# Optimization experiments

Hardware: AMD Instinct MI355X
Metric: run time of the kernel (lower is better)

The kernel has to match this reference:

```python
import jax, jax.numpy as jnp
import numpy as np

GRID = 16
PAD = 32
RADIUS = 8
SIGMA = 1.5
B = 8192
N_SEEDS = 24


def setup_inputs() -> dict:
    key = jax.random.key(0)
    k1, k2 = jax.random.split(key)
    # predicted seeds: (x, y, phase), coords in [0, GRID)
    output = jax.random.uniform(k1, (B, N_SEEDS * 3), dtype=jnp.float32) * GRID
    # target seeds: (x, y, amp), coords in [0, 2*GRID)
    targets = jax.random.uniform(k2, (B, N_SEEDS * 3), dtype=jnp.float32) * (2 * GRID)
    return {"output": output, "targets": targets}


def _forward(output, targets):
    Bn = output.shape[0]
    seeds = output.reshape(Bn, -1, 3)   # (B, N, 3): x, y, phase
    tgt = targets.reshape(Bn, -1, 3)    # (B, M, 3): x, y, amp

    # --- discrete Voronoi on GRID x GRID (vectorized over batch) ---
    c = jnp.arange(GRID, dtype=output.dtype)
    xx, yy = jnp.meshgrid(c, c, indexing='ij')  # (GRID, GRID)
    dist = jnp.sqrt((xx[None, :, :, None] - seeds[:, None, None, :, 0]) ** 2
                    + (yy[None, :, :, None] - seeds[:, None, None, :, 1]) ** 2)
    labels = jnp.argmin(dist, axis=-1)  # (B, GRID, GRID) int

    # circular support on the inner grid (np.ogrid[-r:r, -r:r] convention)
    cc = jnp.arange(-RADIUS, RADIUS)
    inner = (cc[:, None] ** 2 + cc[None, :] ** 2) <= RADIUS ** 2
    labels = jnp.where(inner[None], labels, 0)

    # zero-pad voronoi labels to PAD x PAD
    pw = (PAD - GRID) // 2
    padded = jnp.pad(labels, ((0, 0), (pw, pw), (pw, pw)))  # (B, PAD, PAD)

    # --- gather phase per pixel, zero outside circle on padded grid ---
    phases = seeds[:, :, 2]  # (B, N)
    phase = jnp.take_along_axis(phases, padded.reshape(Bn, -1), axis=1).reshape(Bn, PAD, PAD)
    pc = jnp.arange(PAD)
    center = PAD // 2
    outside = (pc[:, None] - center) ** 2 + (pc[None, :] - center) ** 2 > RADIUS ** 2
    phase = jnp.where(outside[None], jnp.zeros_like(phase), phase)

    # --- density = amp(=1) * exp(i * 2*pi * phase), shifted FFT magnitude ---
    two_pi = 2.0 * jnp.pi
    density = jax.lax.complex(jnp.cos(two_pi * phase), jnp.sin(two_pi * phase))
    pred = jnp.fft.fftshift(density, axes=(-2, -1))
    pred = jnp.fft.fft2(pred)
    pred_dp = jnp.abs(jnp.fft.fftshift(pred, axes=(-2, -1)))  # (B, PAD, PAD)

    # --- target diffraction: sum of Gaussians on (2*GRID)x(2*GRID) grid ---
    xc = jnp.arange(PAD, dtype=targets.dtype)  # height == width == 2*GRID == PAD
    tx = tgt[:, :, 0][:, :, None, None]
    ty = tgt[:, :, 1][:, :, None, None]
    amp = tgt[:, :, 2][:, :, None, None]
    # torch: x varies along last axis, y along second-to-last
    d2 = (xc[None, None, None, :] - tx) ** 2 + (xc[None, None, :, None] - ty) ** 2
    tgt_dp = jnp.sum(amp * jnp.exp(-d2 / (2.0 * SIGMA ** 2)), axis=1)  # (B, PAD, PAD)

    # --- chi-square (global max-normalization and reductions) ---
    p = pred_dp / jnp.max(pred_dp)
    t = tgt_dp / jnp.max(tgt_dp)
    return jnp.sum((p - t) ** 2) / jnp.sqrt(jnp.sum(p ** 2) * jnp.sum(t ** 2))


def reference(output, targets):
    return _forward(output, targets)
```

## Files before the change

kernel.cpp:

```cpp
#include <hip/hip_runtime.h>
#include <math.h>

#define NS 24

typedef float v2f __attribute__((ext_vector_type(2)));
typedef float v4f __attribute__((ext_vector_type(4)));


struct PixTab { unsigned short v[196]; };
__device__ constexpr PixTab make_pix() {
    PixTab t{};
    int n = 0;
    const int w[16] = {0,3,5,6,6,7,7,7,8,7,7,7,6,6,5,3};
    for (int yy = 0; yy < 16; ++yy)
        for (int x = 16 - w[yy]; x <= 16 + w[yy]; ++x)
            if (x < 24) { t.v[n] = (unsigned short)((yy << 8) | x); n = n + 1; }
    t.v[195] = (unsigned short)((8 << 8) | 24);
    return t;
}
__device__ constexpr PixTab PIX = make_pix();

constexpr float twc_(int p) {
    const float C[17] = {
        1.0f, 0.98078528040323044913f, 0.92387953251128675613f, 0.83146961230254523708f,
        0.70710678118654752440f, 0.55557023301960222474f, 0.38268343236508977173f,
        0.19509032201612826785f, 0.0f,
        -0.19509032201612826785f, -0.38268343236508977173f, -0.55557023301960222474f,
        -0.70710678118654752440f, -0.83146961230254523708f, -0.92387953251128675613f,
        -0.98078528040323044913f, -1.0f };
    return (p <= 16) ? C[p] : C[32 - p];
}
constexpr float tws_(int p) {
    const float S[17] = {
        0.0f, 0.19509032201612826785f, 0.38268343236508977173f, 0.55557023301960222474f,
        0.70710678118654752440f, 0.83146961230254523708f, 0.92387953251128675613f,
        0.98078528040323044913f, 1.0f,
        0.98078528040323044913f, 0.92387953251128675613f, 0.83146961230254523708f,
        0.70710678118654752440f, 0.55557023301960222474f, 0.38268343236508977173f,
        0.19509032201612826785f, 0.0f };
    return (p <= 16) ? -S[p] : S[32 - p];
}
struct alignas(16) TW1T { float v[16 * 18 * 2]; };
__device__ constexpr TW1T make_tw1() {
    TW1T t{};
    for (int l0 = 0; l0 < 16; ++l0)
        for (int xp = 0; xp < 17; ++xp) {
            int p = (l0 * (xp + 8)) & 31;
            t.v[(l0 * 18 + xp) * 2 + 0] = twc_(p);
            t.v[(l0 * 18 + xp) * 2 + 1] = tws_(p);
        }
    return t;
}
__device__ constexpr TW1T TW1G = make_tw1();
struct alignas(16) TW2T { float v[8 * 18 * 2]; };
__device__ constexpr TW2T make_tw2() {
    TW2T t{};
    for (int k0 = 0; k0 < 8; ++k0)
        for (int yp = 0; yp < 16; ++yp) {
            int p = (k0 * (yp + 8)) & 31;
            t.v[(k0 * 18 + yp) * 2 + 0] = twc_(p);
            t.v[(k0 * 18 + yp) * 2 + 1] = tws_(p);
        }
    return t;
}
__device__ constexpr TW2T TW2G = make_tw2();

static __device__ __forceinline__ v2f cmul(v2f e, v2f w) {
    v2f m = (v2f){e.y, e.y} * (v2f){w.y, w.x};
    return __builtin_elementwise_fma((v2f){e.x, e.x}, w, (v2f){-m.x, m.y});
}

__global__ __launch_bounds__(256)
void loss_main(const float* __restrict__ output, const float* __restrict__ targets,
               float* __restrict__ partials, int B) {
    __shared__ float2 sxy[NS];
    __shared__ float sp[NS];
    __shared__ float tx[NS], ty[NS], ta[NS];
    __shared__ float2 e24s;
    __shared__ __align__(16) float gx[NS * 32];
    __shared__ __align__(16) float gyT[32 * 24];
    __shared__ __align__(16) float e2f[16 * 18 * 2];
    __shared__ __align__(16) float tw2f[8 * 36];
    __shared__ __align__(16) float gT2f[32 * 36];
    __shared__ __align__(16) char uA[5120];
    __shared__ float redm[4][5];

    float* tw1f = (float*)uA;
    float* pmf  = (float*)uA;

    const int b = blockIdx.x;
    const int t = threadIdx.x;
    const float* so = output + b * NS * 3;
    const float* tg = targets + b * NS * 3;

    if (t < NS) {
        sxy[t] = make_float2(so[3 * t + 0], so[3 * t + 1]);
        sp[t] = so[3 * t + 2];
        if (t == 0) {
            float sv0, cv0;
            __sincosf(6.2831853071795864f * sp[0], &sv0, &cv0);
            e24s = make_float2(cv0 - 1.0f, sv0);
        }
    }
    if (t >= 64 && t < 64 + NS) {
        int s = t - 64;
        tx[s] = tg[3 * s + 0];
        ty[s] = tg[3 * s + 1];
        ta[s] = tg[3 * s + 2];
    }
    if (t < 216) {
        if (t < 144) *(v4f*)&tw1f[t * 4] = *(const v4f*)&TW1G.v[t * 4];
        else         *(v4f*)&tw2f[(t - 144) * 4] = *(const v4f*)&TW2G.v[(t - 144) * 4];
    }
    for (int i = t; i < 16 * 18; i += 256) *(v2f*)&e2f[i * 2] = (v2f){0.f, 0.f};
    __syncthreads();

    for (int idx = t; idx < NS * 32; idx += 256) {
        int s = idx >> 5, c = idx & 31;
        float dx = (float)c - tx[s];
        gx[idx] = ta[s] * __expf(dx * dx * (-1.0f / 4.5f));
    }
    for (int idx = t; idx < 32 * 24; idx += 256) {
        int r = idx / 24, s = idx - r * 24;
        float dy = (float)r - ty[s];
        gyT[idx] = __expf(dy * dy * (-1.0f / 4.5f));
    }

    if (t < 196) {
        int pv = (int)PIX.v[t];
        int yy = pv >> 8, x = pv & 255;
        float ph;
        if (t < 195) {
            float fi = (float)yy, fj = (float)(x - 8);
            int best = 0;
            float bd = 1e30f;
#pragma unroll
            for (int s = 0; s < NS; ++s) {
                float2 sv = sxy[s];
                float ddx = fi - sv.x, ddy = fj - sv.y;
                float d2 = ddx * ddx + ddy * ddy;
                if (d2 < bd) { bd = d2; best = s; }
            }
            ph = sp[best];
        } else {
            ph = sp[0];
        }
        float sv_, cv_;
        __sincosf(6.2831853071795864f * ph, &sv_, &cv_);
        *(v2f*)&e2f[(yy * 18 + (x - 8)) * 2] = (v2f){cv_ - 1.0f, sv_};
    }
    __syncthreads();

    {
        int yy = t >> 4, l0 = t & 15;
        const float* row = &e2f[yy * 36];
        const float* twr = &tw1f[l0 * 36];
        v2f g0 = {0.f, 0.f}, g1 = {0.f, 0.f};
#pragma unroll
        for (int q = 0; q < 8; ++q) {
            v4f e4 = *(const v4f*)&row[q * 4];
            v4f w4 = *(const v4f*)&twr[q * 4];
            v2f ca = cmul((v2f){e4.x, e4.y}, (v2f){w4.x, w4.y});
            v2f cb = cmul((v2f){e4.z, e4.w}, (v2f){w4.z, w4.w});
            g0 += ca + cb;
            g1 += ca - cb;
        }
        {
            v2f e16 = *(const v2f*)&row[32];
            v2f w16 = *(const v2f*)&twr[32];
            v2f c16 = cmul(e16, w16);
            g0 += c16; g1 += c16;
        }
        *(v2f*)&gT2f[l0 * 36 + yy * 2] = g0;
        *(v2f*)&gT2f[(l0 + 16) * 36 + yy * 2] = g1;
    }
    __syncthreads();

    {
        int l = t >> 3, k0 = t & 7;
        const float* gTr = &gT2f[l * 36];
        const float* twr = &tw2f[k0 * 36];
        v2f h0 = {0,0}, h1 = {0,0}, h2 = {0,0}, h3 = {0,0};
#pragma unroll
        for (int q = 0; q < 4; ++q) {
            v4f ga = *(const v4f*)&gTr[q * 8];
            v4f gb = *(const v4f*)&gTr[q * 8 + 4];
            v4f wa = *(const v4f*)&twr[q * 8];
            v4f wb = *(const v4f*)&twr[q * 8 + 4];
            v2f t0 = cmul((v2f){ga.x, ga.y}, (v2f){wa.x, wa.y});
            v2f t1 = cmul((v2f){ga.z, ga.w}, (v2f){wa.z, wa.w});
            v2f t2 = cmul((v2f){gb.x, gb.y}, (v2f){wb.x, wb.y});
            v2f t3 = cmul((v2f){gb.z, gb.w}, (v2f){wb.z, wb.w});
            v2f a = t0 + t2, bb = t0 - t2;
            v2f c = t1 + t3, d = t1 - t3;
            v2f du = {d.y, -d.x};
            h0 += a + c;
            h1 += bb + du;
            h2 += a - c;
            h3 += bb - du;
        }
        {
            float2 e24 = e24s;
            int m = k0 & 3;
            float ar2 = (m == 0) ? 1.f : (m == 2) ? -1.f : 0.f;
            float ai2 = (m == 1) ? 1.f : (m == 3) ? -1.f : 0.f;
            float sgn = (l & 1) ? -1.f : 1.f;
            v2f T = {sgn * (e24.x * ar2 - e24.y * ai2),
                     sgn * (e24.x * ai2 + e24.y * ar2)};
            h0 += T; h1 += T; h2 += T; h3 += T;
        }
        if (t == 0) h0.x += 1024.0f;
        int v = (l + 16) & 31;
        v2f q0 = h0 * h0, q1 = h1 * h1, q2 = h2 * h2, q3 = h3 * h3;
        pmf[((k0 + 16) & 31) * 40 + v] = sqrtf(q0.x + q0.y);
        pmf[((k0 + 24) & 31) * 40 + v] = sqrtf(q1.x + q1.y);
        pmf[(k0)        * 40 + v]      = sqrtf(q2.x + q2.y);
        pmf[(k0 + 8)    * 40 + v]      = sqrtf(q3.x + q3.y);
    }
    __syncthreads();

    float mp, mt, sp2, st2, spt;
    {
        int r = t >> 3;
        int c0 = (t & 7) * 4;
        v4f p4 = *(const v4f*)&pmf[r * 40 + c0];
        v2f t01 = {0.f, 0.f}, t23 = {0.f, 0.f};
#pragma unroll
        for (int q = 0; q < 6; ++q) {
            v4f gy4 = *(const v4f*)&gyT[r * 24 + q * 4];
#pragma unroll
            for (int j = 0; j < 4; ++j) {
                int s = 4 * q + j;
                v4f g4 = *(const v4f*)&gx[s * 32 + c0];
                float gyv = (j == 0) ? gy4.x : (j == 1) ? gy4.y : (j == 2) ? gy4.z : gy4.w;
                v2f gv = {gyv, gyv};
                t01 = __builtin_elementwise_fma(gv, (v2f){g4.x, g4.y}, t01);
                t23 = __builtin_elementwise_fma(gv, (v2f){g4.z, g4.w}, t23);
            }
        }
        v2f p01 = {p4.x, p4.y}, p23 = {p4.z, p4.w};
        v2f s2v = __builtin_elementwise_fma(p23, p23, p01 * p01);
        v2f t2v = __builtin_elementwise_fma(t23, t23, t01 * t01);
        v2f ptv = __builtin_elementwise_fma(p23, t23, p01 * t01);
        sp2 = s2v.x + s2v.y;
        st2 = t2v.x + t2v.y;
        spt = ptv.x + ptv.y;
        mp = fmaxf(fmaxf(p4.x, p4.y), fmaxf(p4.z, p4.w));
        mt = fmaxf(fmaxf(t01.x, t01.y), fmaxf(t23.x, t23.y));
    }

    for (int off = 32; off > 0; off >>= 1) {
        mp  = fmaxf(mp, __shfl_down(mp, off));
        mt  = fmaxf(mt, __shfl_down(mt, off));
        sp2 += __shfl_down(sp2, off);
        st2 += __shfl_down(st2, off);
        spt += __shfl_down(spt, off);
    }
    int wave = t >> 6, lane = t & 63;
    if (lane == 0) {
        redm[wave][0] = sp2; redm[wave][1] = st2; redm[wave][2] = spt;
        redm[wave][3] = mp;  redm[wave][4] = mt;
    }
    __syncthreads();
    if (t == 0) {
        for (int w = 1; w < 4; ++w) {
            sp2 += redm[w][0];
            st2 += redm[w][1];
            spt += redm[w][2];
            mp = fmaxf(mp, redm[w][3]);
            mt = fmaxf(mt, redm[w][4]);
        }
        partials[0 * B + b] = sp2;
        partials[1 * B + b] = st2;
        partials[2 * B + b] = spt;
        partials[3 * B + b] = mp;
        partials[4 * B + b] = mt;
    }
}

__global__ __launch_bounds__(1024)
void finalize_loss(const float* __restrict__ partials, float* __restrict__ out, int B) {
    __shared__ double reds[16][3];
    __shared__ float redx[16][2];
    const int t = threadIdx.x;
    double sp2 = 0.0, st2 = 0.0, spt = 0.0;
    float mp = 0.f, mt = 0.f;
    for (int i = t; i < B; i += 1024) {
        sp2 += (double)partials[0 * B + i];
        st2 += (double)partials[1 * B + i];
        spt += (double)partials[2 * B + i];
        mp = fmaxf(mp, partials[3 * B + i]);
        mt = fmaxf(mt, partials[4 * B + i]);
    }
    for (int off = 32; off > 0; off >>= 1) {
        sp2 += __shfl_down(sp2, off);
        st2 += __shfl_down(st2, off);
        spt += __shfl_down(spt, off);
        mp = fmaxf(mp, __shfl_down(mp, off));
        mt = fmaxf(mt, __shfl_down(mt, off));
    }
    int wave = t >> 6, lane = t & 63;
    if (lane == 0) {
        reds[wave][0] = sp2; reds[wave][1] = st2; reds[wave][2] = spt;
        redx[wave][0] = mp;  redx[wave][1] = mt;
    }
    __syncthreads();
    if (t == 0) {
        for (int w = 1; w < 16; ++w) {
            sp2 += reds[w][0];
            st2 += reds[w][1];
            spt += reds[w][2];
            mp = fmaxf(mp, redx[w][0]);
            mt = fmaxf(mt, redx[w][1]);
        }
        double Mp = (double)mp, Mt = (double)mt;
        double loss = (sp2 * (Mt / Mp) + st2 * (Mp / Mt) - 2.0 * spt) / sqrt(sp2 * st2);
        out[0] = (float)loss;
    }
}

extern "C" void kernel_launch(void* const* d_in, const int* in_sizes, int n_in,
                              void* d_out, int out_size, void* d_ws, size_t ws_size,
                              hipStream_t stream) {
    const float* output  = (const float*)d_in[0];
    const float* targets = (const float*)d_in[1];
    int B = in_sizes[0] / (NS * 3);
    float* partials = (float*)d_ws;

    loss_main<<<B, 256, 0, stream>>>(output, targets, partials, B);
    finalize_loss<<<1, 1024, 0, stream>>>(partials, (float*)d_out, B);
}
```

Baseline: 102.9 us.

## Use deeper radix splits in both FFT stages to halve twiddle work

Restructures the two DFT stages so each thread computes more outputs through extra in-register butterfly levels: radix-4 outputs in the first pass and radix-8 in the second. Twiddle tables shrink by half, and only 128 threads do the FFT work instead of 256. This cuts complex multiplies and twiddle loads from shared memory. In exchange, per-thread register use and serial work go up, and half the block sits idle during these phases.

```diff
diff --git a/kernel.cpp b/kernel.cpp
--- a/kernel.cpp
+++ b/kernel.cpp
@@ -40,22 +40,22 @@
         0.19509032201612826785f, 0.0f };
     return (p <= 16) ? -S[p] : S[32 - p];
 }
-struct alignas(16) TW1T { float v[16 * 18 * 2]; };
+struct alignas(16) TW1T { float v[8 * 18 * 2]; };
 __device__ constexpr TW1T make_tw1() {
     TW1T t{};
-    for (int l0 = 0; l0 < 16; ++l0)
-        for (int xp = 0; xp < 17; ++xp) {
-            int p = (l0 * (xp + 8)) & 31;
-            t.v[(l0 * 18 + xp) * 2 + 0] = twc_(p);
-            t.v[(l0 * 18 + xp) * 2 + 1] = tws_(p);
+    for (int l0 = 0; l0 < 8; ++l0)
+        for (int xi = 0; xi < 17; ++xi) {
+            int p = (l0 * (xi + 8)) & 31;
+            t.v[(l0 * 18 + xi) * 2 + 0] = twc_(p);
+            t.v[(l0 * 18 + xi) * 2 + 1] = tws_(p);
         }
     return t;
 }
 __device__ constexpr TW1T TW1G = make_tw1();
-struct alignas(16) TW2T { float v[8 * 18 * 2]; };
+struct alignas(16) TW2T { float v[4 * 18 * 2]; };
 __device__ constexpr TW2T make_tw2() {
     TW2T t{};
-    for (int k0 = 0; k0 < 8; ++k0)
+    for (int k0 = 0; k0 < 4; ++k0)
         for (int yp = 0; yp < 16; ++yp) {
             int p = (k0 * (yp + 8)) & 31;
             t.v[(k0 * 18 + yp) * 2 + 0] = twc_(p);
@@ -68,6 +68,10 @@
 static __device__ __forceinline__ v2f cmul(v2f e, v2f w) {
     v2f m = (v2f){e.y, e.y} * (v2f){w.y, w.x};
     return __builtin_elementwise_fma((v2f){e.x, e.x}, w, (v2f){-m.x, m.y});
+}
+static __device__ __forceinline__ float mag(v2f h) {
+    v2f q = h * h;
+    return sqrtf(q.x + q.y);
 }
 
 __global__ __launch_bounds__(256)
@@ -80,7 +84,7 @@
     __shared__ __align__(16) float gx[NS * 32];
     __shared__ __align__(16) float gyT[32 * 24];
     __shared__ __align__(16) float e2f[16 * 18 * 2];
-    __shared__ __align__(16) float tw2f[8 * 36];
+    __shared__ __align__(16) float tw2f[4 * 36];
     __shared__ __align__(16) float gT2f[32 * 36];
     __shared__ __align__(16) char uA[5120];
     __shared__ float redm[4][5];
@@ -108,9 +112,9 @@
         ty[s] = tg[3 * s + 1];
         ta[s] = tg[3 * s + 2];
     }
-    if (t < 216) {
-        if (t < 144) *(v4f*)&tw1f[t * 4] = *(const v4f*)&TW1G.v[t * 4];
-        else         *(v4f*)&tw2f[(t - 144) * 4] = *(const v4f*)&TW2G.v[(t - 144) * 4];
+    if (t < 108) {
+        if (t < 72) *(v4f*)&tw1f[t * 4] = *(const v4f*)&TW1G.v[t * 4];
+        else        *(v4f*)&tw2f[(t - 72) * 4] = *(const v4f*)&TW2G.v[(t - 72) * 4];
     }
     for (int i = t; i < 16 * 18; i += 256) *(v2f*)&e2f[i * 2] = (v2f){0.f, 0.f};
     __syncthreads();
@@ -151,79 +155,91 @@
     }
     __syncthreads();
 
-    {
-        int yy = t >> 4, l0 = t & 15;
+    if (t < 128) {
+        int yy = t >> 3, l0 = t & 7;
         const float* row = &e2f[yy * 36];
         const float* twr = &tw1f[l0 * 36];
-        v2f g0 = {0.f, 0.f}, g1 = {0.f, 0.f};
+        v2f c0 = {0,0}, c1 = {0,0}, c2 = {0,0}, c3 = {0,0};
 #pragma unroll
         for (int q = 0; q < 8; ++q) {
             v4f e4 = *(const v4f*)&row[q * 4];
             v4f w4 = *(const v4f*)&twr[q * 4];
             v2f ca = cmul((v2f){e4.x, e4.y}, (v2f){w4.x, w4.y});
             v2f cb = cmul((v2f){e4.z, e4.w}, (v2f){w4.z, w4.w});
-            g0 += ca + cb;
-            g1 += ca - cb;
+            if ((q & 1) == 0) { c0 += ca; c1 += cb; }
+            else              { c2 += ca; c3 += cb; }
         }
         {
             v2f e16 = *(const v2f*)&row[32];
             v2f w16 = *(const v2f*)&twr[32];
-            v2f c16 = cmul(e16, w16);
-            g0 += c16; g1 += c16;
-        }
-        *(v2f*)&gT2f[l0 * 36 + yy * 2] = g0;
-        *(v2f*)&gT2f[(l0 + 16) * 36 + yy * 2] = g1;
-    }
-    __syncthreads();
-
-    {
-        int l = t >> 3, k0 = t & 7;
+            c0 += cmul(e16, w16);
+        }
+        v2f a = c0 + c2, bb = c0 - c2;
+        v2f cc = c1 + c3, d = c1 - c3;
+        v2f du = {d.y, -d.x};
+        *(v2f*)&gT2f[l0 * 36 + yy * 2]        = a + cc;
+        *(v2f*)&gT2f[(l0 + 8) * 36 + yy * 2]  = bb + du;
+        *(v2f*)&gT2f[(l0 + 16) * 36 + yy * 2] = a - cc;
+        *(v2f*)&gT2f[(l0 + 24) * 36 + yy * 2] = bb - du;
+    }
+    __syncthreads();
+
+    if (t < 128) {
+        int l = t >> 2, k0 = t & 3;
         const float* gTr = &gT2f[l * 36];
         const float* twr = &tw2f[k0 * 36];
-        v2f h0 = {0,0}, h1 = {0,0}, h2 = {0,0}, h3 = {0,0};
+        v2f c[8];
 #pragma unroll
         for (int q = 0; q < 4; ++q) {
-            v4f ga = *(const v4f*)&gTr[q * 8];
-            v4f gb = *(const v4f*)&gTr[q * 8 + 4];
-            v4f wa = *(const v4f*)&twr[q * 8];
-            v4f wb = *(const v4f*)&twr[q * 8 + 4];
-            v2f t0 = cmul((v2f){ga.x, ga.y}, (v2f){wa.x, wa.y});
-            v2f t1 = cmul((v2f){ga.z, ga.w}, (v2f){wa.z, wa.w});
-            v2f t2 = cmul((v2f){gb.x, gb.y}, (v2f){wb.x, wb.y});
-            v2f t3 = cmul((v2f){gb.z, gb.w}, (v2f){wb.z, wb.w});
-            v2f a = t0 + t2, bb = t0 - t2;
-            v2f c = t1 + t3, d = t1 - t3;
-            v2f du = {d.y, -d.x};
-            h0 += a + c;
-            h1 += bb + du;
-            h2 += a - c;
-            h3 += bb - du;
-        }
+            v4f glo = *(const v4f*)&gTr[q * 4];
+            v4f ghi = *(const v4f*)&gTr[q * 4 + 16];
+            v4f wlo = *(const v4f*)&twr[q * 4];
+            v4f whi = *(const v4f*)&twr[q * 4 + 16];
+            c[2 * q]     = cmul((v2f){glo.x, glo.y}, (v2f){wlo.x, wlo.y})
+                         + cmul((v2f){ghi.x, ghi.y}, (v2f){whi.x, whi.y});
+            c[2 * q + 1] = cmul((v2f){glo.z, glo.w}, (v2f){wlo.z, wlo.w})
+                         + cmul((v2f){ghi.z, ghi.w}, (v2f){whi.z, whi.w});
+        }
+        v2f Ea = c[0] + c[4], Eb = c[0] - c[4];
+        v2f Ec = c[2] + c[6], Ed = c[2] - c[6];
+        v2f Edu = {Ed.y, -Ed.x};
+        v2f E0 = Ea + Ec, E1 = Eb + Edu, E2 = Ea - Ec, E3 = Eb - Edu;
+        v2f Oa = c[1] + c[5], Ob = c[1] - c[5];
+        v2f Oc = c[3] + c[7], Od = c[3] - c[7];
+        v2f Odu = {Od.y, -Od.x};
+        v2f O0 = Oa + Oc, O1 = Ob + Odu, O2 = Oa - Oc, O3 = Ob - Odu;
+        const float s2 = 0.70710678118654752440f;
+        v2f w1O = (v2f){s2, s2} * (v2f){O1.x + O1.y, O1.y - O1.x};
+        v2f w3O = (v2f){s2, s2} * (v2f){O3.y - O3.x, -(O3.x + O3.y)};
+        v2f miO = {O2.y, -O2.x};
         {
             float2 e24 = e24s;
-            int m = k0 & 3;
-            float ar2 = (m == 0) ? 1.f : (m == 2) ? -1.f : 0.f;
-            float ai2 = (m == 1) ? 1.f : (m == 3) ? -1.f : 0.f;
+            float ar2 = (k0 == 0) ? 1.f : (k0 == 2) ? -1.f : 0.f;
+            float ai2 = (k0 == 1) ? 1.f : (k0 == 3) ? -1.f : 0.f;
             float sgn = (l & 1) ? -1.f : 1.f;
             v2f T = {sgn * (e24.x * ar2 - e24.y * ai2),
                      sgn * (e24.x * ai2 + e24.y * ar2)};
-            h0 += T; h1 += T; h2 += T; h3 += T;
-        }
+            E0 += T; E1 += T; E2 += T; E3 += T;
+        }
+        v2f h0 = E0 + O0;
         if (t == 0) h0.x += 1024.0f;
         int v = (l + 16) & 31;
-        v2f q0 = h0 * h0, q1 = h1 * h1, q2 = h2 * h2, q3 = h3 * h3;
-        pmf[((k0 + 16) & 31) * 40 + v] = sqrtf(q0.x + q0.y);
-        pmf[((k0 + 24) & 31) * 40 + v] = sqrtf(q1.x + q1.y);
-        pmf[(k0)        * 40 + v]      = sqrtf(q2.x + q2.y);
-        pmf[(k0 + 8)    * 40 + v]      = sqrtf(q3.x + q3.y);
+        pmf[(k0 + 16) * 40 + v] = mag(h0);
+        pmf[(k0 + 20) * 40 + v] = mag(E1 + w1O);
+        pmf[(k0 + 24) * 40 + v] = mag(E2 + miO);
+        pmf[(k0 + 28) * 40 + v] = mag(E3 + w3O);
+        pmf[(k0)      * 40 + v] = mag(E0 - O0);
+        pmf[(k0 + 4)  * 40 + v] = mag(E1 - w1O);
+        pmf[(k0 + 8)  * 40 + v] = mag(E2 - miO);
+        pmf[(k0 + 12) * 40 + v] = mag(E3 - w3O);
     }
     __syncthreads();
 
     float mp, mt, sp2, st2, spt;
     {
         int r = t >> 3;
-        int c0 = (t & 7) * 4;
-        v4f p4 = *(const v4f*)&pmf[r * 40 + c0];
+        int c0i = (t & 7) * 4;
+        v4f p4 = *(const v4f*)&pmf[r * 40 + c0i];
         v2f t01 = {0.f, 0.f}, t23 = {0.f, 0.f};
 #pragma unroll
         for (int q = 0; q < 6; ++q) {
@@ -231,7 +247,7 @@
 #pragma unroll
             for (int j = 0; j < 4; ++j) {
                 int s = 4 * q + j;
-                v4f g4 = *(const v4f*)&gx[s * 32 + c0];
+                v4f g4 = *(const v4f*)&gx[s * 32 + c0i];
                 float gyv = (j == 0) ? gy4.x : (j == 1) ? gy4.y : (j == 2) ? gy4.z : gy4.w;
                 v2f gv = {gyv, gyv};
                 t01 = __builtin_elementwise_fma(gv, (v2f){g4.x, g4.y}, t01);
```

Measured after the change: 98.38 us. 4.4% less time.
